# Optimization experiments

Measured on AMD Instinct MI355X. Metric: run time of the kernel, lower is better.

## Reference

```python
import jax, jax.numpy as jnp
import numpy as np
from jax.scipy.special import logsumexp

REG = 1.0
N_ITER = 50  # fixed Sinkhorn iterations (log-domain, stabilized)


def setup_inputs() -> dict:
    key = jax.random.key(0)
    k1, k2 = jax.random.split(key)
    source = jax.random.normal(k1, (8192, 256), dtype=jnp.float32)
    target = jax.random.normal(k2, (8192, 256), dtype=jnp.float32)
    return {"source": source, "target": target}


def _sinkhorn_value(x, y, reg):
    # squared euclidean cost matrix [n, m]
    M = (jnp.sum(x * x, axis=1)[:, None]
         + jnp.sum(y * y, axis=1)[None, :]
         - 2.0 * (x @ y.T))
    n, m = M.shape
    loga = -jnp.log(jnp.float32(n))  # uniform weights
    logb = -jnp.log(jnp.float32(m))
    Mr = M / reg

    def step(fg, _):
        f, g = fg
        # f_i = -reg * logsumexp_j((g_j - M_ij)/reg + log b_j)
        f = -reg * logsumexp(g[None, :] / reg - Mr + logb, axis=1)
        g = -reg * logsumexp(f[:, None] / reg - Mr + loga, axis=0)
        return (f, g), None

    f0 = jnp.zeros((n,), dtype=M.dtype)
    g0 = jnp.zeros((m,), dtype=M.dtype)
    (f, g), _ = jax.lax.scan(step, (f0, g0), None, length=N_ITER)

    # log P_ij = (f_i + g_j - M_ij)/reg + log a_i + log b_j
    logP = (f[:, None] + g[None, :]) / reg - Mr + (loga + logb)
    P = jnp.exp(logP)
    value_linear = jnp.sum(P * M)
    # KL(P || a x b) entropic term (reg_type='KL' default in POT)
    kl = jnp.sum(P * (logP - loga - logb))
    return value_linear + reg * kl


def reference(source, target):
    value = _sinkhorn_value(source, target, REG)
    return jnp.sqrt(value)
```

## Files before the change

kernel.cpp:

```cpp
#include <hip/hip_runtime.h>

#define N 8192
#define DK 256
#define LOG2E 1.4426950408889634f
#define LN2   0.6931471805599453f
#define ZS    2.5f
#define QS    1.1541560327f
#define BIAS  320.0f

typedef unsigned short u16;
typedef u16   ushort8 __attribute__((ext_vector_type(8)));
typedef __bf16 bf16x8 __attribute__((ext_vector_type(8)));
typedef float  f32x4  __attribute__((ext_vector_type(4)));

__device__ __forceinline__ u16 f2bf(float f){
  unsigned u = __builtin_bit_cast(unsigned, f);
  return (u16)((u + 0x7fffu + ((u >> 16) & 1u)) >> 16);
}
__device__ __forceinline__ float ex2(float x){
  float r; asm("v_exp_f32 %0, %1" : "=v"(r) : "v"(x)); return r;
}
__device__ __forceinline__ float lg2(float x){
  float r; asm("v_log_f32 %0, %1" : "=v"(r) : "v"(x)); return r;
}
__device__ __forceinline__ float cub0(unsigned u){ float r; asm("v_cvt_f32_ubyte0 %0, %1":"=v"(r):"v"(u)); return r; }
__device__ __forceinline__ float cub1(unsigned u){ float r; asm("v_cvt_f32_ubyte1 %0, %1":"=v"(r):"v"(u)); return r; }
__device__ __forceinline__ float cub2(unsigned u){ float r; asm("v_cvt_f32_ubyte2 %0, %1":"=v"(r):"v"(u)); return r; }
__device__ __forceinline__ float cub3(unsigned u){ float r; asm("v_cvt_f32_ubyte3 %0, %1":"=v"(r):"v"(u)); return r; }

__global__ __launch_bounds__(256) void prep_k(const float* __restrict__ x, const float* __restrict__ y,
                                              u16* __restrict__ xb, u16* __restrict__ yb,
                                              float* __restrict__ x2, float* __restrict__ y2,
                                              float* __restrict__ gts){
  const int w = threadIdx.x >> 6, l = threadIdx.x & 63;
  const int r = blockIdx.x * 4 + w;
  const bool isx = r < N;
  const int rr = isx ? r : r - N;
  const float* src = (isx ? x : y) + (size_t)rr * DK;
  float4 v = *(const float4*)(src + l * 4);
  ushort4 bv;
  bv.x = f2bf(v.x); bv.y = f2bf(v.y); bv.z = f2bf(v.z); bv.w = f2bf(v.w);
  *(ushort4*)((isx ? xb : yb) + (size_t)rr * DK + l * 4) = bv;
  float p = v.x*v.x + v.y*v.y + v.z*v.z + v.w*v.w;
  #pragma unroll
  for (int off = 32; off > 0; off >>= 1) p += __shfl_down(p, off);
  if (l == 0){
    if (isx) x2[rr] = p;
    else { y2[rr] = p; gts[rr] = -p * LOG2E - BIAS; }
  }
}

__global__ __launch_bounds__(256) void gemm_k(const u16* __restrict__ xb, const u16* __restrict__ yb,
                                              unsigned char* __restrict__ zq,
                                              unsigned char* __restrict__ zqT){
  __shared__ __align__(16) u16 As[128 * 72];
  __shared__ __align__(16) u16 Bs[128 * 72];
  const int t = threadIdx.x;
  const int w = t >> 6, l = t & 63;
  const int wm = w >> 1, wn = w & 1;
  const int brow = blockIdx.y * 128, bcol = blockIdx.x * 128;
  const int tr = t >> 3, tc = t & 7;
  f32x4 acc[4][4] = {};
  for (int ks = 0; ks < 4; ++ks){
    #pragma unroll
    for (int rr = 0; rr < 4; ++rr){
      const int row = tr + rr * 32;
      *(ushort8*)&As[row * 72 + tc * 8] = *(const ushort8*)&xb[(size_t)(brow + row) * DK + ks * 64 + tc * 8];
      *(ushort8*)&Bs[row * 72 + tc * 8] = *(const ushort8*)&yb[(size_t)(bcol + row) * DK + ks * 64 + tc * 8];
    }
    __syncthreads();
    #pragma unroll
    for (int kk = 0; kk < 2; ++kk){
      bf16x8 av[4], bv[4];
      #pragma unroll
      for (int mi = 0; mi < 4; ++mi){
        const int ar = wm * 64 + mi * 16 + (l & 15);
        av[mi] = __builtin_bit_cast(bf16x8, *(const ushort8*)&As[ar * 72 + kk * 32 + (l >> 4) * 8]);
      }
      #pragma unroll
      for (int ni = 0; ni < 4; ++ni){
        const int br = wn * 64 + ni * 16 + (l & 15);
        bv[ni] = __builtin_bit_cast(bf16x8, *(const ushort8*)&Bs[br * 72 + kk * 32 + (l >> 4) * 8]);
      }
      #pragma unroll
      for (int mi = 0; mi < 4; ++mi)
        #pragma unroll
        for (int ni = 0; ni < 4; ++ni)
          acc[mi][ni] = __builtin_amdgcn_mfma_f32_16x16x32_bf16(av[mi], bv[ni], acc[mi][ni], 0, 0, 0);
    }
    __syncthreads();
  }
  unsigned char* Cs = (unsigned char*)As;
  unsigned char* Ct = (unsigned char*)Bs;
  #pragma unroll
  for (int mi = 0; mi < 4; ++mi){
    const int rowb = wm * 64 + mi * 16 + (l >> 4) * 4;
    #pragma unroll
    for (int ni = 0; ni < 4; ++ni){
      const int col = wn * 64 + ni * 16 + (l & 15);
      unsigned pk = 0;
      #pragma unroll
      for (int rr = 0; rr < 4; ++rr){
        float q = fminf(fmaxf(acc[mi][ni][rr] * QS, -127.f), 127.f);
        unsigned b = (unsigned)((int)__builtin_rintf(q) + 128) & 255u;
        Cs[(rowb + rr) * 128 + col] = (unsigned char)b;
        pk |= b << (8 * rr);
      }
      *(unsigned*)(Ct + col * 144 + rowb) = pk;
    }
  }
  __syncthreads();
  const int trow0 = t >> 3, kseg = t & 7;
  #pragma unroll
  for (int ii = 0; ii < 4; ++ii){
    const int row = trow0 + ii * 32;
    int4 v = *(const int4*)(Cs + row * 128 + kseg * 16);
    *(int4*)(zq + (size_t)(brow + row) * N + bcol + kseg * 16) = v;
    int4 vt = *(const int4*)(Ct + row * 144 + kseg * 16);
    *(int4*)(zqT + (size_t)(bcol + row) * N + brow + kseg * 16) = vt;
  }
}

template<int MODE>
__global__ __launch_bounds__(256) void sweep_k(const unsigned char* __restrict__ z,
                                               const float* __restrict__ din,
                                               float* __restrict__ dout,
                                               const float* __restrict__ fprev,
                                               const float* __restrict__ x2,
                                               float* __restrict__ contrib){
  const int w = threadIdx.x >> 6, l = threadIdx.x & 63;
  const int i = blockIdx.x * 4 + w;
  const unsigned char* zr = z + (size_t)i * N + l * 16;
  float m = -1e30f, s = 0.f;
  uint4 zA = *(const uint4*)(zr);
  #pragma unroll
  for (int it = 0; it < 8; ++it){
    uint4 zB = {};
    if (it < 7) zB = *(const uint4*)(zr + (it + 1) * 1024);
    const float* gp = din + it * 1024 + l * 16;
    const float4 g0 = *(const float4*)(gp);
    const float4 g1 = *(const float4*)(gp + 4);
    const float4 g2 = *(const float4*)(gp + 8);
    const float4 g3 = *(const float4*)(gp + 12);
    float tt[16];
    tt[0]  = __builtin_fmaf(cub0(zA.x), ZS, g0.x);
    tt[1]  = __builtin_fmaf(cub1(zA.x), ZS, g0.y);
    tt[2]  = __builtin_fmaf(cub2(zA.x), ZS, g0.z);
    tt[3]  = __builtin_fmaf(cub3(zA.x), ZS, g0.w);
    tt[4]  = __builtin_fmaf(cub0(zA.y), ZS, g1.x);
    tt[5]  = __builtin_fmaf(cub1(zA.y), ZS, g1.y);
    tt[6]  = __builtin_fmaf(cub2(zA.y), ZS, g1.z);
    tt[7]  = __builtin_fmaf(cub3(zA.y), ZS, g1.w);
    tt[8]  = __builtin_fmaf(cub0(zA.z), ZS, g2.x);
    tt[9]  = __builtin_fmaf(cub1(zA.z), ZS, g2.y);
    tt[10] = __builtin_fmaf(cub2(zA.z), ZS, g2.z);
    tt[11] = __builtin_fmaf(cub3(zA.z), ZS, g2.w);
    tt[12] = __builtin_fmaf(cub0(zA.w), ZS, g3.x);
    tt[13] = __builtin_fmaf(cub1(zA.w), ZS, g3.y);
    tt[14] = __builtin_fmaf(cub2(zA.w), ZS, g3.z);
    tt[15] = __builtin_fmaf(cub3(zA.w), ZS, g3.w);
    float a0 = fmaxf(tt[0], tt[1]),  a1 = fmaxf(tt[2], tt[3]);
    float a2 = fmaxf(tt[4], tt[5]),  a3 = fmaxf(tt[6], tt[7]);
    float a4 = fmaxf(tt[8], tt[9]),  a5 = fmaxf(tt[10], tt[11]);
    float a6 = fmaxf(tt[12], tt[13]), a7 = fmaxf(tt[14], tt[15]);
    float b0 = fmaxf(a0, a1), b1 = fmaxf(a2, a3), b2 = fmaxf(a4, a5), b3 = fmaxf(a6, a7);
    float nm = fmaxf(fmaxf(fmaxf(b0, b1), fmaxf(b2, b3)), m);
    float s0 = ex2(tt[0] - nm) + ex2(tt[1] - nm) + ex2(tt[2] - nm) + ex2(tt[3] - nm)
             + ex2(tt[4] - nm) + ex2(tt[5] - nm) + ex2(tt[6] - nm) + ex2(tt[7] - nm);
    float s1 = ex2(tt[8] - nm) + ex2(tt[9] - nm) + ex2(tt[10] - nm) + ex2(tt[11] - nm)
             + ex2(tt[12] - nm) + ex2(tt[13] - nm) + ex2(tt[14] - nm) + ex2(tt[15] - nm);
    s = __builtin_fmaf(s, ex2(m - nm), s0 + s1);
    m = nm;
    zA = zB;
  }
  #pragma unroll
  for (int off = 32; off > 0; off >>= 1){
    float om = __shfl_down(m, off);
    float os = __shfl_down(s, off);
    float nm = fmaxf(m, om);
    s = __builtin_fmaf(s, ex2(m - nm), os * ex2(om - nm));
    m = nm;
  }
  if (l == 0){
    float lse2 = m + lg2(s);
    if (MODE == 0){
      dout[i] = 13.0f - lse2 - BIAS;
    } else {
      float fti = fprev[i] + BIAS;
      float r = ex2(fti + lse2 - 26.0f);
      contrib[i] = (fti * LN2 + x2[i]) * r;
    }
  }
}

__global__ __launch_bounds__(256) void finish_k(const float* __restrict__ contrib,
                                                const float* __restrict__ gts,
                                                const float* __restrict__ y2,
                                                float* __restrict__ out){
  __shared__ float s1[256], s2[256];
  const int t = threadIdx.x;
  float a = 0.f, b = 0.f;
  for (int j = t; j < N; j += 256){ a += contrib[j]; b += (gts[j] + BIAS) * LN2 + y2[j]; }
  s1[t] = a; s2[t] = b; __syncthreads();
  for (int st = 128; st > 0; st >>= 1){
    if (t < st){ s1[t] += s1[t + st]; s2[t] += s2[t + st]; }
    __syncthreads();
  }
  if (t == 0) out[0] = sqrtf(s1[0] + s2[0] * (1.0f / (float)N));
}

extern "C" void kernel_launch(void* const* d_in, const int* in_sizes, int n_in,
                              void* d_out, int out_size, void* d_ws, size_t ws_size,
                              hipStream_t stream){
  const float* x = (const float*)d_in[0];
  const float* y = (const float*)d_in[1];
  float* out = (float*)d_out;
  char* ws = (char*)d_ws;

  unsigned char* zq  = (unsigned char*)(ws);
  unsigned char* zqT = (unsigned char*)(ws + 67108864);
  u16*   xb      = (u16*)  (ws + 134217728);
  u16*   yb      = (u16*)  (ws + 138412032);
  float* x2      = (float*)(ws + 142606336);
  float* y2      = (float*)(ws + 142639104);
  float* fts     = (float*)(ws + 142671872);
  float* gts     = (float*)(ws + 142704640);
  float* contrib = (float*)(ws + 142737408);

  prep_k<<<4096, 256, 0, stream>>>(x, y, xb, yb, x2, y2, gts);
  gemm_k<<<dim3(64, 64), 256, 0, stream>>>(xb, yb, zq, zqT);
  for (int it = 0; it < 50; ++it){
    sweep_k<0><<<2048, 256, 0, stream>>>(zq,  gts, fts, nullptr, nullptr, nullptr);
    sweep_k<0><<<2048, 256, 0, stream>>>(zqT, fts, gts, nullptr, nullptr, nullptr);
  }
  sweep_k<1><<<2048, 256, 0, stream>>>(zq, gts, nullptr, fts, x2, contrib);
  finish_k<<<1, 256, 0, stream>>>(contrib, gts, y2, out);
}
```

Before: 2.030 ms.

## Use previous-iteration LSE as fixed max to skip online max in Sinkhorn sweeps

```diff
diff --git a/kernel.cpp b/kernel.cpp
--- a/kernel.cpp
+++ b/kernel.cpp
@@ -27,6 +27,14 @@
 __device__ __forceinline__ float cub1(unsigned u){ float r; asm("v_cvt_f32_ubyte1 %0, %1":"=v"(r):"v"(u)); return r; }
 __device__ __forceinline__ float cub2(unsigned u){ float r; asm("v_cvt_f32_ubyte2 %0, %1":"=v"(r):"v"(u)); return r; }
 __device__ __forceinline__ float cub3(unsigned u){ float r; asm("v_cvt_f32_ubyte3 %0, %1":"=v"(r):"v"(u)); return r; }
+
+__device__ __forceinline__ float quad(unsigned u, float4 gv, float M){
+  float t0 = __builtin_fmaf(cub0(u), ZS, gv.x - M);
+  float t1 = __builtin_fmaf(cub1(u), ZS, gv.y - M);
+  float t2 = __builtin_fmaf(cub2(u), ZS, gv.z - M);
+  float t3 = __builtin_fmaf(cub3(u), ZS, gv.w - M);
+  return (ex2(t0) + ex2(t1)) + (ex2(t2) + ex2(t3));
+}
 
 __global__ __launch_bounds__(256) void prep_k(const float* __restrict__ x, const float* __restrict__ y,
                                               u16* __restrict__ xb, u16* __restrict__ yb,
@@ -121,13 +129,10 @@
   }
 }
 
-template<int MODE>
-__global__ __launch_bounds__(256) void sweep_k(const unsigned char* __restrict__ z,
-                                               const float* __restrict__ din,
-                                               float* __restrict__ dout,
-                                               const float* __restrict__ fprev,
-                                               const float* __restrict__ x2,
-                                               float* __restrict__ contrib){
+__global__ __launch_bounds__(256) void sweept_k(const unsigned char* __restrict__ z,
+                                                const float* __restrict__ din,
+                                                float* __restrict__ dout,
+                                                float* __restrict__ pmax_out){
   const int w = threadIdx.x >> 6, l = threadIdx.x & 63;
   const int i = blockIdx.x * 4 + w;
   const unsigned char* zr = z + (size_t)i * N + l * 16;
@@ -135,7 +140,7 @@
   uint4 zA = *(const uint4*)(zr);
   #pragma unroll
   for (int it = 0; it < 8; ++it){
-    uint4 zB = {};
+    uint4 zB = zA;
     if (it < 7) zB = *(const uint4*)(zr + (it + 1) * 1024);
     const float* gp = din + it * 1024 + l * 16;
     const float4 g0 = *(const float4*)(gp);
@@ -183,12 +188,69 @@
   }
   if (l == 0){
     float lse2 = m + lg2(s);
+    dout[i] = 13.0f - lse2 - BIAS;
+    pmax_out[i] = lse2;
+  }
+}
+
+template<int MODE>
+__global__ __launch_bounds__(256, 8) void sweepf_k(const unsigned char* __restrict__ z,
+                                                   const float* __restrict__ din,
+                                                   float* __restrict__ dout,
+                                                   const float* __restrict__ pmax_in,
+                                                   float* __restrict__ pmax_out,
+                                                   const float* __restrict__ fprev,
+                                                   const float* __restrict__ x2,
+                                                   float* __restrict__ contrib){
+  const int w = threadIdx.x >> 6, l = threadIdx.x & 63;
+  const int p = w & 1, h = w >> 1;
+  const int r0 = blockIdx.x * 4;
+  const int i0 = r0 + 2 * p, i1 = i0 + 1;
+  const float M0 = pmax_in[i0], M1 = pmax_in[i1];
+  const int cbase = h * 4096 + l * 16;
+  const unsigned char* z0 = z + (size_t)i0 * N + cbase;
+  const unsigned char* z1 = z + (size_t)i1 * N + cbase;
+  float s0 = 0.f, s1 = 0.f;
+  uint4 a0 = *(const uint4*)z0;
+  uint4 a1 = *(const uint4*)z1;
+  #pragma unroll
+  for (int it = 0; it < 4; ++it){
+    uint4 b0 = a0, b1 = a1;
+    if (it < 3){
+      b0 = *(const uint4*)(z0 + (it + 1) * 1024);
+      b1 = *(const uint4*)(z1 + (it + 1) * 1024);
+    }
+    const float* gp = din + h * 4096 + it * 1024 + l * 16;
+    const float4 g0 = *(const float4*)(gp);
+    const float4 g1 = *(const float4*)(gp + 4);
+    const float4 g2 = *(const float4*)(gp + 8);
+    const float4 g3 = *(const float4*)(gp + 12);
+    s0 += (quad(a0.x, g0, M0) + quad(a0.y, g1, M0))
+        + (quad(a0.z, g2, M0) + quad(a0.w, g3, M0));
+    s1 += (quad(a1.x, g0, M1) + quad(a1.y, g1, M1))
+        + (quad(a1.z, g2, M1) + quad(a1.w, g3, M1));
+    a0 = b0; a1 = b1;
+  }
+  #pragma unroll
+  for (int off = 32; off > 0; off >>= 1){
+    s0 += __shfl_down(s0, off);
+    s1 += __shfl_down(s1, off);
+  }
+  __shared__ float sB[4][2];
+  if (l == 0){ sB[2 * p + 0][h] = s0; sB[2 * p + 1][h] = s1; }
+  __syncthreads();
+  if (threadIdx.x < 4){
+    const int row = r0 + threadIdx.x;
+    float s = sB[threadIdx.x][0] + sB[threadIdx.x][1];
+    float M = pmax_in[row];
+    float lse = M + lg2(s);
     if (MODE == 0){
-      dout[i] = 13.0f - lse2 - BIAS;
+      dout[row] = 13.0f - lse - BIAS;
+      pmax_out[row] = lse;
     } else {
-      float fti = fprev[i] + BIAS;
-      float r = ex2(fti + lse2 - 26.0f);
-      contrib[i] = (fti * LN2 + x2[i]) * r;
+      float fti = fprev[row] + BIAS;
+      float r = ex2(fti + lse - 26.0f);
+      contrib[row] = (fti * LN2 + x2[row]) * r;
     }
   }
 }
@@ -226,13 +288,19 @@
   float* fts     = (float*)(ws + 142671872);
   float* gts     = (float*)(ws + 142704640);
   float* contrib = (float*)(ws + 142737408);
+  float* pmaxF   = (float*)(ws + 142770176);
+  float* pmaxG   = (float*)(ws + 142802944);
 
   prep_k<<<4096, 256, 0, stream>>>(x, y, xb, yb, x2, y2, gts);
   gemm_k<<<dim3(64, 64), 256, 0, stream>>>(xb, yb, zq, zqT);
-  for (int it = 0; it < 50; ++it){
-    sweep_k<0><<<2048, 256, 0, stream>>>(zq,  gts, fts, nullptr, nullptr, nullptr);
-    sweep_k<0><<<2048, 256, 0, stream>>>(zqT, fts, gts, nullptr, nullptr, nullptr);
-  }
-  sweep_k<1><<<2048, 256, 0, stream>>>(zq, gts, nullptr, fts, x2, contrib);
+  for (int it = 0; it < 3; ++it){
+    sweept_k<<<2048, 256, 0, stream>>>(zq,  gts, fts, pmaxF);
+    sweept_k<<<2048, 256, 0, stream>>>(zqT, fts, gts, pmaxG);
+  }
+  for (int it = 3; it < 50; ++it){
+    sweepf_k<0><<<2048, 256, 0, stream>>>(zq,  gts, fts, pmaxF, pmaxF, nullptr, nullptr, nullptr);
+    sweepf_k<0><<<2048, 256, 0, stream>>>(zqT, fts, gts, pmaxG, pmaxG, nullptr, nullptr, nullptr);
+  }
+  sweepf_k<1><<<2048, 256, 0, stream>>>(zq, gts, nullptr, pmaxF, nullptr, fts, x2, contrib);
   finish_k<<<1, 256, 0, stream>>>(contrib, gts, y2, out);
 }
```

Result: faster. 1.645 ms (-19.0%).

## Sort potentials and skip negligible column blocks via per-block max bounds

Applied to the files above, without the earlier changes.

```diff
diff --git a/kernel.cpp b/kernel.cpp
--- a/kernel.cpp
+++ b/kernel.cpp
@@ -27,6 +27,15 @@
 __device__ __forceinline__ float cub1(unsigned u){ float r; asm("v_cvt_f32_ubyte1 %0, %1":"=v"(r):"v"(u)); return r; }
 __device__ __forceinline__ float cub2(unsigned u){ float r; asm("v_cvt_f32_ubyte2 %0, %1":"=v"(r):"v"(u)); return r; }
 __device__ __forceinline__ float cub3(unsigned u){ float r; asm("v_cvt_f32_ubyte3 %0, %1":"=v"(r):"v"(u)); return r; }
+
+__device__ __forceinline__ unsigned fkey(float f){
+  unsigned b = __float_as_uint(f);
+  return (b & 0x80000000u) ? ~b : (b | 0x80000000u);
+}
+__device__ __forceinline__ float fdec(unsigned k){
+  unsigned b = (k & 0x80000000u) ? (k ^ 0x80000000u) : ~k;
+  return __uint_as_float(b);
+}
 
 __global__ __launch_bounds__(256) void prep_k(const float* __restrict__ x, const float* __restrict__ y,
                                               u16* __restrict__ xb, u16* __restrict__ yb,
@@ -48,6 +57,10 @@
     if (isx) x2[rr] = p;
     else { y2[rr] = p; gts[rr] = -p * LOG2E - BIAS; }
   }
+}
+
+__global__ __launch_bounds__(256) void zero_k(unsigned* __restrict__ g){
+  g[blockIdx.x * 256 + threadIdx.x] = 0u;
 }
 
 __global__ __launch_bounds__(256) void gemm_k(const u16* __restrict__ xb, const u16* __restrict__ yb,
@@ -121,13 +134,10 @@
   }
 }
 
-template<int MODE>
-__global__ __launch_bounds__(256) void sweep_k(const unsigned char* __restrict__ z,
-                                               const float* __restrict__ din,
-                                               float* __restrict__ dout,
-                                               const float* __restrict__ fprev,
-                                               const float* __restrict__ x2,
-                                               float* __restrict__ contrib){
+__global__ __launch_bounds__(256) void sweept_k(const unsigned char* __restrict__ z,
+                                                const float* __restrict__ din,
+                                                float* __restrict__ dout,
+                                                float* __restrict__ pmax_out){
   const int w = threadIdx.x >> 6, l = threadIdx.x & 63;
   const int i = blockIdx.x * 4 + w;
   const unsigned char* zr = z + (size_t)i * N + l * 16;
@@ -135,7 +145,7 @@
   uint4 zA = *(const uint4*)(zr);
   #pragma unroll
   for (int it = 0; it < 8; ++it){
-    uint4 zB = {};
+    uint4 zB = zA;
     if (it < 7) zB = *(const uint4*)(zr + (it + 1) * 1024);
     const float* gp = din + it * 1024 + l * 16;
     const float4 g0 = *(const float4*)(gp);
@@ -183,12 +193,150 @@
   }
   if (l == 0){
     float lse2 = m + lg2(s);
+    dout[i] = 13.0f - lse2 - BIAS;
+    pmax_out[i] = lse2;
+  }
+}
+
+__global__ __launch_bounds__(256) void rank_k(const float* __restrict__ key,
+                                              int* __restrict__ src){
+  const int j = blockIdx.x * 256 + threadIdx.x;
+  const float v = key[j];
+  int r = 0;
+  for (int jj = 0; jj < N; jj += 4){
+    const float4 k4 = *(const float4*)(key + jj);
+    r += (k4.x < v) || (k4.x == v && (jj + 0) < j);
+    r += (k4.y < v) || (k4.y == v && (jj + 1) < j);
+    r += (k4.z < v) || (k4.z == v && (jj + 2) < j);
+    r += (k4.w < v) || (k4.w == v && (jj + 3) < j);
+  }
+  src[r] = j;
+}
+
+__global__ __launch_bounds__(256) void repackz_k(unsigned char* __restrict__ zq,
+                                                 unsigned char* __restrict__ zqT,
+                                                 const int* __restrict__ srcG,
+                                                 const int* __restrict__ srcF,
+                                                 unsigned char* __restrict__ maxqF,
+                                                 unsigned char* __restrict__ maxqG){
+  __shared__ __align__(16) unsigned char orig[8192];
+  __shared__ __align__(16) unsigned char sorted[8192];
+  const int side = blockIdx.x >> 13;
+  const int row  = blockIdx.x & 8191;
+  unsigned char* z = side ? zqT : zq;
+  const int* srcC  = side ? srcF : srcG;
+  unsigned char* mq = side ? maxqG : maxqF;
+  unsigned char* zr = z + (size_t)row * N;
+  const int t = threadIdx.x;
+  #pragma unroll
+  for (int k = 0; k < 2; ++k)
+    *(uint4*)(orig + t * 16 + k * 4096) = *(const uint4*)(zr + t * 16 + k * 4096);
+  __syncthreads();
+  #pragma unroll
+  for (int k = 0; k < 8; ++k){
+    const int d = t + k * 256;
+    const int4 sc = *(const int4*)(srcC + d * 4);
+    unsigned b0 = orig[sc.x], b1 = orig[sc.y], b2 = orig[sc.z], b3 = orig[sc.w];
+    *(unsigned*)(sorted + d * 4) = b0 | (b1 << 8) | (b2 << 16) | (b3 << 24);
+  }
+  __syncthreads();
+  #pragma unroll
+  for (int k = 0; k < 2; ++k)
+    *(uint4*)(zr + t * 16 + k * 4096) = *(const uint4*)(sorted + t * 16 + k * 4096);
+  if (t < 128){
+    const unsigned char* p = sorted + t * 64;
+    unsigned mx = 0;
+    #pragma unroll
+    for (int d = 0; d < 16; ++d){
+      unsigned u = *(const unsigned*)(p + d * 4);
+      unsigned a = u & 255u, b = (u >> 8) & 255u, c = (u >> 16) & 255u, e = u >> 24;
+      mx = mx > a ? mx : a; mx = mx > b ? mx : b;
+      mx = mx > c ? mx : c; mx = mx > e ? mx : e;
+    }
+    mq[(size_t)row * 128 + t] = (unsigned char)mx;
+  }
+}
+
+__global__ __launch_bounds__(256) void repackd_k(const int* __restrict__ srcF, const int* __restrict__ srcG,
+    const float* __restrict__ fts, const float* __restrict__ gts,
+    const float* __restrict__ pmaxF, const float* __restrict__ pmaxG,
+    const float* __restrict__ x2, const float* __restrict__ y2,
+    float* __restrict__ fts_p, float* __restrict__ gts_p,
+    float* __restrict__ pmaxF_p, float* __restrict__ pmaxG_p,
+    float* __restrict__ x2p, float* __restrict__ y2p,
+    unsigned* __restrict__ gmax6){
+  const int r = blockIdx.x * 256 + threadIdx.x;
+  const int sf = srcF[r], sg = srcG[r];
+  fts_p[r] = fts[sf]; pmaxF_p[r] = pmaxF[sf]; x2p[r] = x2[sf];
+  const float gv = gts[sg];
+  gts_p[r] = gv; pmaxG_p[r] = pmaxG[sg]; y2p[r] = y2[sg];
+  atomicMax(gmax6 + (r >> 6), fkey(gv));
+}
+
+template<int MODE>
+__global__ __launch_bounds__(256, 8) void sweeps_k(
+    const unsigned char* __restrict__ z,
+    const unsigned char* __restrict__ maxq,
+    const int* __restrict__ srcRow,
+    const float* __restrict__ din,
+    const unsigned* __restrict__ gmax_in,
+    float* __restrict__ dout,
+    unsigned* __restrict__ gmax_out,
+    const float* __restrict__ pmax_in,
+    float* __restrict__ pmax_out,
+    const float* __restrict__ fprev,
+    const float* __restrict__ x2,
+    float* __restrict__ contrib,
+    float CUT){
+  __shared__ unsigned short lists[4][128];
+  const int w = threadIdx.x >> 6, l = threadIdx.x & 63;
+  const int r = blockIdx.x * 4 + w;
+  const int prow = srcRow[r];
+  const float M = pmax_in[r];
+  const unsigned char* mqp = maxq + (size_t)prow * 128;
+  const float thr = M - CUT;
+  const float b0 = __builtin_fmaf((float)mqp[l],      ZS, fdec(gmax_in[l]));
+  const float b1 = __builtin_fmaf((float)mqp[l + 64], ZS, fdec(gmax_in[l + 64]));
+  const bool sv0 = b0 > thr, sv1 = b1 > thr;
+  const unsigned long long m0 = __ballot(sv0), m1 = __ballot(sv1);
+  const int S0 = __popcll(m0);
+  int S = S0 + __popcll(m1);
+  const unsigned long long low = (1ull << l) - 1ull;
+  if (sv0) lists[w][__popcll(m0 & low)] = (unsigned short)l;
+  if (sv1) lists[w][S0 + __popcll(m1 & low)] = (unsigned short)(l + 64);
+  if (S == 0){ if (l == 0) lists[w][0] = 0; S = 1; }
+  const unsigned char* zr = z + (size_t)prow * N + l;
+  const float* dg = din + l;
+  float s = 0.f;
+  for (int k = 0; k < S; k += 8){
+    unsigned q0[8]; float g0[8];
+    #pragma unroll
+    for (int j = 0; j < 8; ++j){
+      int kk = k + j; kk = kk < S ? kk : S - 1;
+      const int c = ((int)lists[w][kk]) << 6;
+      q0[j] = zr[c];
+      g0[j] = dg[c];
+    }
+    #pragma unroll
+    for (int j = 0; j < 8; ++j){
+      float t = __builtin_fmaf((float)q0[j], ZS, g0[j] - M);
+      float e = ex2(t);
+      s += (k + j < S) ? e : 0.f;
+    }
+  }
+  #pragma unroll
+  for (int off = 32; off > 0; off >>= 1) s += __shfl_down(s, off);
+  if (l == 0){
+    const float lse = M + lg2(s);
     if (MODE == 0){
-      dout[i] = 13.0f - lse2 - BIAS;
+      const float dv = 13.0f - lse - BIAS;
+      dout[r] = dv;
+      pmax_out[r] = lse;
+      atomicMax(gmax_out + (r >> 6), fkey(dv));
     } else {
-      float fti = fprev[i] + BIAS;
-      float r = ex2(fti + lse2 - 26.0f);
-      contrib[i] = (fti * LN2 + x2[i]) * r;
+      const float fti = fprev[r] + BIAS;
+      const float rr = ex2(fti + lse - 26.0f);
+      contrib[r] = (fti * LN2 + x2[r]) * rr;
     }
   }
 }
@@ -217,22 +365,54 @@
   float* out = (float*)d_out;
   char* ws = (char*)d_ws;
 
-  unsigned char* zq  = (unsigned char*)(ws);
-  unsigned char* zqT = (unsigned char*)(ws + 67108864);
-  u16*   xb      = (u16*)  (ws + 134217728);
-  u16*   yb      = (u16*)  (ws + 138412032);
-  float* x2      = (float*)(ws + 142606336);
-  float* y2      = (float*)(ws + 142639104);
-  float* fts     = (float*)(ws + 142671872);
-  float* gts     = (float*)(ws + 142704640);
-  float* contrib = (float*)(ws + 142737408);
-
+  unsigned char* zq    = (unsigned char*)(ws);
+  unsigned char* zqT   = (unsigned char*)(ws + 67108864);
+  u16*   xb     = (u16*)  (ws + 134217728);
+  u16*   yb     = (u16*)  (ws + 138412032);
+  unsigned char* maxqF = (unsigned char*)(ws + 142606336);
+  unsigned char* maxqG = (unsigned char*)(ws + 143654912);
+  char* fb = ws + 144703488;
+  float* x2      = (float*)(fb);
+  float* y2      = (float*)(fb + 32768);
+  float* fts     = (float*)(fb + 65536);
+  float* gts     = (float*)(fb + 98304);
+  float* pmaxF   = (float*)(fb + 131072);
+  float* pmaxG   = (float*)(fb + 163840);
+  float* fts_p   = (float*)(fb + 196608);
+  float* gts_p   = (float*)(fb + 229376);
+  float* pmaxF_p = (float*)(fb + 262144);
+  float* pmaxG_p = (float*)(fb + 294912);
+  float* x2p     = (float*)(fb + 327680);
+  float* y2p     = (float*)(fb + 360448);
+  float* contrib = (float*)(fb + 393216);
+  int*   srcF    = (int*)  (fb + 425984);
+  int*   srcG    = (int*)  (fb + 458752);
+  unsigned* gmax = (unsigned*)(fb + 491520);
+
+  zero_k<<<52, 256, 0, stream>>>(gmax);
   prep_k<<<4096, 256, 0, stream>>>(x, y, xb, yb, x2, y2, gts);
   gemm_k<<<dim3(64, 64), 256, 0, stream>>>(xb, yb, zq, zqT);
-  for (int it = 0; it < 50; ++it){
-    sweep_k<0><<<2048, 256, 0, stream>>>(zq,  gts, fts, nullptr, nullptr, nullptr);
-    sweep_k<0><<<2048, 256, 0, stream>>>(zqT, fts, gts, nullptr, nullptr, nullptr);
-  }
-  sweep_k<1><<<2048, 256, 0, stream>>>(zq, gts, nullptr, fts, x2, contrib);
-  finish_k<<<1, 256, 0, stream>>>(contrib, gts, y2, out);
-}
+  for (int it = 0; it < 3; ++it){
+    sweept_k<<<2048, 256, 0, stream>>>(zq,  gts, fts, pmaxF);
+    sweept_k<<<2048, 256, 0, stream>>>(zqT, fts, gts, pmaxG);
+  }
+  rank_k<<<32, 256, 0, stream>>>(fts, srcF);
+  rank_k<<<32, 256, 0, stream>>>(gts, srcG);
+  repackz_k<<<16384, 256, 0, stream>>>(zq, zqT, srcG, srcF, maxqF, maxqG);
+  repackd_k<<<32, 256, 0, stream>>>(srcF, srcG, fts, gts, pmaxF, pmaxG, x2, y2,
+                                    fts_p, gts_p, pmaxF_p, pmaxG_p, x2p, y2p,
+                                    gmax + 6 * 128);
+  for (int s = 6; s < 100; s += 2){
+    const float cut = (s == 6) ? 70.0f : 45.0f;
+    sweeps_k<0><<<2048, 256, 0, stream>>>(zq,  maxqF, srcF, gts_p, gmax + s * 128,
+                                          fts_p, gmax + (s + 1) * 128,
+                                          pmaxF_p, pmaxF_p, nullptr, nullptr, nullptr, cut);
+    sweeps_k<0><<<2048, 256, 0, stream>>>(zqT, maxqG, srcG, fts_p, gmax + (s + 1) * 128,
+                                          gts_p, gmax + (s + 2) * 128,
+                                          pmaxG_p, pmaxG_p, nullptr, nullptr, nullptr, cut);
+  }
+  sweeps_k<1><<<2048, 256, 0, stream>>>(zq, maxqF, srcF, gts_p, gmax + 100 * 128,
+                                        nullptr, nullptr, pmaxF_p, nullptr,
+                                        fts_p, x2p, contrib, 45.0f);
+  finish_k<<<1, 256, 0, stream>>>(contrib, gts_p, y2p, out);
+}
```

Result: slower. 4.374 ms (+115.5%).

## Skip negligible 64-column blocks in Sinkhorn sweeps using per-block max bounds

Applied to the files above, without the earlier changes.

```diff
diff --git a/kernel.cpp b/kernel.cpp
--- a/kernel.cpp
+++ b/kernel.cpp
@@ -27,6 +27,16 @@
 __device__ __forceinline__ float cub1(unsigned u){ float r; asm("v_cvt_f32_ubyte1 %0, %1":"=v"(r):"v"(u)); return r; }
 __device__ __forceinline__ float cub2(unsigned u){ float r; asm("v_cvt_f32_ubyte2 %0, %1":"=v"(r):"v"(u)); return r; }
 __device__ __forceinline__ float cub3(unsigned u){ float r; asm("v_cvt_f32_ubyte3 %0, %1":"=v"(r):"v"(u)); return r; }
+
+__device__ __forceinline__ unsigned fkey(float f){
+  unsigned b = __float_as_uint(f);
+  return (b & 0x80000000u) ? ~b : (b | 0x80000000u);
+}
+__device__ __forceinline__ float fdec(unsigned k){
+  unsigned b = (k & 0x80000000u) ? (k ^ 0x80000000u) : ~k;
+  return __uint_as_float(b);
+}
+__device__ __forceinline__ unsigned umax2(unsigned a, unsigned b){ return a > b ? a : b; }
 
 __global__ __launch_bounds__(256) void prep_k(const float* __restrict__ x, const float* __restrict__ y,
                                               u16* __restrict__ xb, u16* __restrict__ yb,
@@ -50,9 +60,15 @@
   }
 }
 
+__global__ __launch_bounds__(256) void zero_k(unsigned* __restrict__ g){
+  g[blockIdx.x * 256 + threadIdx.x] = 0u;
+}
+
 __global__ __launch_bounds__(256) void gemm_k(const u16* __restrict__ xb, const u16* __restrict__ yb,
                                               unsigned char* __restrict__ zq,
-                                              unsigned char* __restrict__ zqT){
+                                              unsigned char* __restrict__ zqT,
+                                              unsigned char* __restrict__ maxqF,
+                                              unsigned char* __restrict__ maxqG){
   __shared__ __align__(16) u16 As[128 * 72];
   __shared__ __align__(16) u16 Bs[128 * 72];
   const int t = threadIdx.x;
@@ -92,6 +108,14 @@
   }
   unsigned char* Cs = (unsigned char*)As;
   unsigned char* Ct = (unsigned char*)Bs;
+  unsigned umf[4][4];
+  unsigned umt[4];
+  #pragma unroll
+  for (int mi = 0; mi < 4; ++mi)
+    #pragma unroll
+    for (int rr = 0; rr < 4; ++rr) umf[mi][rr] = 0u;
+  #pragma unroll
+  for (int ni = 0; ni < 4; ++ni) umt[ni] = 0u;
   #pragma unroll
   for (int mi = 0; mi < 4; ++mi){
     const int rowb = wm * 64 + mi * 16 + (l >> 4) * 4;
@@ -105,9 +129,31 @@
         unsigned b = (unsigned)((int)__builtin_rintf(q) + 128) & 255u;
         Cs[(rowb + rr) * 128 + col] = (unsigned char)b;
         pk |= b << (8 * rr);
+        umf[mi][rr] = umax2(umf[mi][rr], b);
+        umt[ni] = umax2(umt[ni], b);
       }
       *(unsigned*)(Ct + col * 144 + rowb) = pk;
     }
+  }
+  #pragma unroll
+  for (int mi = 0; mi < 4; ++mi)
+    #pragma unroll
+    for (int rr = 0; rr < 4; ++rr){
+      unsigned v = umf[mi][rr];
+      v = umax2(v, (unsigned)__shfl_xor((int)v, 1));
+      v = umax2(v, (unsigned)__shfl_xor((int)v, 2));
+      v = umax2(v, (unsigned)__shfl_xor((int)v, 4));
+      v = umax2(v, (unsigned)__shfl_xor((int)v, 8));
+      if ((l & 15) == 0)
+        maxqF[(size_t)(brow + wm * 64 + mi * 16 + (l >> 4) * 4 + rr) * 128 + (bcol >> 6) + wn] = (unsigned char)v;
+    }
+  #pragma unroll
+  for (int ni = 0; ni < 4; ++ni){
+    unsigned v = umt[ni];
+    v = umax2(v, (unsigned)__shfl_xor((int)v, 16));
+    v = umax2(v, (unsigned)__shfl_xor((int)v, 32));
+    if ((l >> 4) == 0)
+      maxqG[(size_t)(bcol + wn * 64 + ni * 16 + (l & 15)) * 128 + (brow >> 6) + wm] = (unsigned char)v;
   }
   __syncthreads();
   const int trow0 = t >> 3, kseg = t & 7;
@@ -121,13 +167,11 @@
   }
 }
 
-template<int MODE>
-__global__ __launch_bounds__(256) void sweep_k(const unsigned char* __restrict__ z,
-                                               const float* __restrict__ din,
-                                               float* __restrict__ dout,
-                                               const float* __restrict__ fprev,
-                                               const float* __restrict__ x2,
-                                               float* __restrict__ contrib){
+__global__ __launch_bounds__(256) void sweept_k(const unsigned char* __restrict__ z,
+                                                const float* __restrict__ din,
+                                                float* __restrict__ dout,
+                                                float* __restrict__ pmax_out,
+                                                unsigned* __restrict__ gmax_out){
   const int w = threadIdx.x >> 6, l = threadIdx.x & 63;
   const int i = blockIdx.x * 4 + w;
   const unsigned char* zr = z + (size_t)i * N + l * 16;
@@ -135,7 +179,7 @@
   uint4 zA = *(const uint4*)(zr);
   #pragma unroll
   for (int it = 0; it < 8; ++it){
-    uint4 zB = {};
+    uint4 zB = zA;
     if (it < 7) zB = *(const uint4*)(zr + (it + 1) * 1024);
     const float* gp = din + it * 1024 + l * 16;
     const float4 g0 = *(const float4*)(gp);
@@ -183,12 +227,74 @@
   }
   if (l == 0){
     float lse2 = m + lg2(s);
+    const float dv = 13.0f - lse2 - BIAS;
+    dout[i] = dv;
+    pmax_out[i] = lse2;
+    atomicMax(gmax_out + (i >> 6), fkey(dv));
+  }
+}
+
+template<int MODE>
+__global__ __launch_bounds__(256) void sweeps_k(
+    const unsigned char* __restrict__ z,
+    const unsigned char* __restrict__ maxq,
+    const float* __restrict__ din,
+    const unsigned* __restrict__ gmax_in,
+    float* __restrict__ dout,
+    unsigned* __restrict__ gmax_out,
+    const float* __restrict__ pmax_in,
+    float* __restrict__ pmax_out,
+    const float* __restrict__ fprev,
+    const float* __restrict__ x2,
+    float* __restrict__ contrib,
+    float CUT){
+  __shared__ unsigned short lists[4][128];
+  const int w = threadIdx.x >> 6, l = threadIdx.x & 63;
+  const int r = blockIdx.x * 4 + w;
+  const float M = pmax_in[r];
+  const unsigned char* mqp = maxq + (size_t)r * 128;
+  const float thr = M - CUT;
+  const float b0 = __builtin_fmaf((float)mqp[l],      ZS, fdec(gmax_in[l]));
+  const float b1 = __builtin_fmaf((float)mqp[l + 64], ZS, fdec(gmax_in[l + 64]));
+  const bool sv0 = b0 > thr, sv1 = b1 > thr;
+  const unsigned long long m0 = __ballot(sv0), m1 = __ballot(sv1);
+  const int S0 = __popcll(m0);
+  int S = S0 + __popcll(m1);
+  const unsigned long long low = (1ull << l) - 1ull;
+  if (sv0) lists[w][__popcll(m0 & low)] = (unsigned short)l;
+  if (sv1) lists[w][S0 + __popcll(m1 & low)] = (unsigned short)(l + 64);
+  if (S == 0){ if (l == 0) lists[w][0] = 0; S = 1; }
+  const unsigned* zr4 = (const unsigned*)(z + (size_t)r * N);
+  const int sub = l >> 4, q16 = l & 15;
+  float s = 0.f;
+  #pragma unroll 2
+  for (int k = 0; k < S; k += 4){
+    int kk = k + sub;
+    const bool act = kk < S;
+    kk = act ? kk : S - 1;
+    const int c = (int)lists[w][kk];
+    const unsigned zd = zr4[c * 16 + q16];
+    const float4 gv = *(const float4*)(din + (c << 6) + (q16 << 2));
+    const float t0 = __builtin_fmaf(cub0(zd), ZS, gv.x - M);
+    const float t1 = __builtin_fmaf(cub1(zd), ZS, gv.y - M);
+    const float t2 = __builtin_fmaf(cub2(zd), ZS, gv.z - M);
+    const float t3 = __builtin_fmaf(cub3(zd), ZS, gv.w - M);
+    const float e = (ex2(t0) + ex2(t1)) + (ex2(t2) + ex2(t3));
+    s += act ? e : 0.f;
+  }
+  #pragma unroll
+  for (int off = 32; off > 0; off >>= 1) s += __shfl_down(s, off);
+  if (l == 0){
+    const float lse = M + lg2(s);
     if (MODE == 0){
-      dout[i] = 13.0f - lse2 - BIAS;
+      const float dv = 13.0f - lse - BIAS;
+      dout[r] = dv;
+      pmax_out[r] = lse;
+      atomicMax(gmax_out + (r >> 6), fkey(dv));
     } else {
-      float fti = fprev[i] + BIAS;
-      float r = ex2(fti + lse2 - 26.0f);
-      contrib[i] = (fti * LN2 + x2[i]) * r;
+      const float fti = fprev[r] + BIAS;
+      const float rr = ex2(fti + lse - 26.0f);
+      contrib[r] = (fti * LN2 + x2[r]) * rr;
     }
   }
 }
@@ -217,22 +323,42 @@
   float* out = (float*)d_out;
   char* ws = (char*)d_ws;
 
-  unsigned char* zq  = (unsigned char*)(ws);
-  unsigned char* zqT = (unsigned char*)(ws + 67108864);
-  u16*   xb      = (u16*)  (ws + 134217728);
-  u16*   yb      = (u16*)  (ws + 138412032);
-  float* x2      = (float*)(ws + 142606336);
-  float* y2      = (float*)(ws + 142639104);
-  float* fts     = (float*)(ws + 142671872);
-  float* gts     = (float*)(ws + 142704640);
-  float* contrib = (float*)(ws + 142737408);
-
+  unsigned char* zq    = (unsigned char*)(ws);
+  unsigned char* zqT   = (unsigned char*)(ws + 67108864);
+  u16*   xb     = (u16*)  (ws + 134217728);
+  u16*   yb     = (u16*)  (ws + 138412032);
+  unsigned char* maxqF = (unsigned char*)(ws + 142606336);
+  unsigned char* maxqG = (unsigned char*)(ws + 143654912);
+  char* fb = ws + 144703488;
+  float* x2      = (float*)(fb);
+  float* y2      = (float*)(fb + 32768);
+  float* fts     = (float*)(fb + 65536);
+  float* gts     = (float*)(fb + 98304);
+  float* pmaxF   = (float*)(fb + 131072);
+  float* pmaxG   = (float*)(fb + 163840);
+  float* contrib = (float*)(fb + 196608);
+  unsigned* gmax = (unsigned*)(fb + 229376);
+
+  zero_k<<<51, 256, 0, stream>>>(gmax);
   prep_k<<<4096, 256, 0, stream>>>(x, y, xb, yb, x2, y2, gts);
-  gemm_k<<<dim3(64, 64), 256, 0, stream>>>(xb, yb, zq, zqT);
-  for (int it = 0; it < 50; ++it){
-    sweep_k<0><<<2048, 256, 0, stream>>>(zq,  gts, fts, nullptr, nullptr, nullptr);
-    sweep_k<0><<<2048, 256, 0, stream>>>(zqT, fts, gts, nullptr, nullptr, nullptr);
-  }
-  sweep_k<1><<<2048, 256, 0, stream>>>(zq, gts, nullptr, fts, x2, contrib);
+  gemm_k<<<dim3(64, 64), 256, 0, stream>>>(xb, yb, zq, zqT, maxqF, maxqG);
+  sweept_k<<<2048, 256, 0, stream>>>(zq,  gts, fts, pmaxF, gmax + 1 * 128);
+  sweept_k<<<2048, 256, 0, stream>>>(zqT, fts, gts, pmaxG, gmax + 2 * 128);
+  sweept_k<<<2048, 256, 0, stream>>>(zq,  gts, fts, pmaxF, gmax + 3 * 128);
+  sweept_k<<<2048, 256, 0, stream>>>(zqT, fts, gts, pmaxG, gmax + 4 * 128);
+  for (int s = 4; s < 100; ++s){
+    const float cut = (s < 6) ? 70.0f : 45.0f;
+    if ((s & 1) == 0)
+      sweeps_k<0><<<2048, 256, 0, stream>>>(zq,  maxqF, gts, gmax + s * 128,
+                                            fts, gmax + (s + 1) * 128,
+                                            pmaxF, pmaxF, nullptr, nullptr, nullptr, cut);
+    else
+      sweeps_k<0><<<2048, 256, 0, stream>>>(zqT, maxqG, fts, gmax + s * 128,
+                                            gts, gmax + (s + 1) * 128,
+                                            pmaxG, pmaxG, nullptr, nullptr, nullptr, cut);
+  }
+  sweeps_k<1><<<2048, 256, 0, stream>>>(zq, maxqF, gts, gmax + 100 * 128,
+                                        nullptr, nullptr, pmaxF, nullptr,
+                                        fts, x2, contrib, 45.0f);
   finish_k<<<1, 256, 0, stream>>>(contrib, gts, y2, out);
 }
```

After: 3.093 ms. 1.52x slower.
